# Optimization experiments

Hardware: AMD Instinct MI355X
Metric: run time of the kernel (lower is better)

Reference implementation:

```python
import jax, jax.numpy as jnp
import numpy as np


def setup_inputs() -> dict:
    key = jax.random.key(0)
    k1, k2, k3 = jax.random.split(key, 3)
    B, Cin, Cout, K, H, W = 32, 128, 128, 4, 112, 112
    x = jax.random.normal(k1, (B, Cin, H, W), dtype=jnp.float32)
    # Conv2d 1x1 weights: [K, out_ch, in_ch] (kernel dims of size 1 squeezed)
    expert_w = jax.random.normal(k2, (K, Cout, Cin), dtype=jnp.float32) * (1.0 / np.sqrt(Cin))
    gate_w = jax.random.normal(k3, (K, Cin), dtype=jnp.float32) * (1.0 / np.sqrt(Cin))
    gate_b = jnp.zeros((K,), dtype=jnp.float32)
    return {"x": x, "expert_w": expert_w, "gate_w": gate_w, "gate_b": gate_b}


def reference(x, expert_w, gate_w, gate_b):
    # Gate: global average pool -> 1x1 conv -> softmax over K
    pooled = jnp.mean(x, axis=(2, 3))                      # [B, Cin]
    logits = pooled @ gate_w.T + gate_b                    # [B, K]
    g = jax.nn.softmax(logits, axis=1)                     # [B, K]
    # Combine expert weights per sample (math-equivalent to sum_k g_k * conv_k(x))
    w_b = jnp.einsum('bk,koi->boi', g, expert_w)           # [B, Cout, Cin]
    out = jnp.einsum('boi,bihw->bohw', w_b, x)             # [B, Cout, H, W]
    return out
```

## Files before the change

### kernel.cpp

```cpp
#include <hip/hip_runtime.h>
#include <hip/hip_bf16.h>
#include <stdint.h>

#define B_    32
#define CIN   128
#define COUT  128
#define KEXP  4
#define HW_   12544

typedef __attribute__((ext_vector_type(8))) short bf16x8;
typedef __attribute__((ext_vector_type(4))) float f32x4;

static __device__ __forceinline__ short f2bf(float f) {
    uint32_t u = __builtin_bit_cast(uint32_t, f);
    u += 0x7FFFu + ((u >> 16) & 1u);
    return (short)(u >> 16);
}

__global__ __launch_bounds__(256) void pool_kernel(const float* __restrict__ x,
                                                   float* __restrict__ pooled) {
    const int row = blockIdx.x;
    const float4* __restrict__ x4 = (const float4*)(x + (size_t)row * HW_);
    const int t = threadIdx.x;
    float s = 0.f;
    for (int idx = t; idx < HW_ / 4; idx += 256) {
        float4 v = x4[idx];
        s += (v.x + v.y) + (v.z + v.w);
    }
    #pragma unroll
    for (int off = 32; off > 0; off >>= 1) s += __shfl_down(s, off, 64);
    __shared__ float wsum[4];
    if ((t & 63) == 0) wsum[t >> 6] = s;
    __syncthreads();
    if (t == 0) pooled[row] = (wsum[0] + wsum[1] + wsum[2] + wsum[3]) * (1.0f / HW_);
}

__global__ __launch_bounds__(256) void gate_kernel(const float* __restrict__ pooled,
                                                   const float* __restrict__ gate_w,
                                                   const float* __restrict__ gate_b,
                                                   const float* __restrict__ expert_w,
                                                   short* __restrict__ wmix) {
    const int b = blockIdx.x;
    const int t = threadIdx.x;
    const int wid = t >> 6, lane = t & 63;
    __shared__ float logits[KEXP];
    __shared__ float gsh[KEXP];
    {
        float p0 = pooled[b * CIN + lane];
        float p1 = pooled[b * CIN + 64 + lane];
        float s = p0 * gate_w[wid * CIN + lane] + p1 * gate_w[wid * CIN + 64 + lane];
        #pragma unroll
        for (int off = 32; off > 0; off >>= 1) s += __shfl_down(s, off, 64);
        if (lane == 0) logits[wid] = s + gate_b[wid];
    }
    __syncthreads();
    if (t == 0) {
        float m = fmaxf(fmaxf(logits[0], logits[1]), fmaxf(logits[2], logits[3]));
        float e0 = expf(logits[0] - m), e1 = expf(logits[1] - m);
        float e2 = expf(logits[2] - m), e3 = expf(logits[3] - m);
        float inv = 1.f / (e0 + e1 + e2 + e3);
        gsh[0] = e0 * inv; gsh[1] = e1 * inv; gsh[2] = e2 * inv; gsh[3] = e3 * inv;
    }
    __syncthreads();
    const float g0 = gsh[0], g1 = gsh[1], g2 = gsh[2], g3 = gsh[3];
    for (int idx = t; idx < COUT * CIN; idx += 256) {
        float w = g0 * expert_w[idx]
                + g1 * expert_w[COUT * CIN + idx]
                + g2 * expert_w[2 * COUT * CIN + idx]
                + g3 * expert_w[3 * COUT * CIN + idx];
        wmix[b * COUT * CIN + idx] = f2bf(w);
    }
}

__global__ __launch_bounds__(256) void conv_kernel(const float* __restrict__ x,
                                                   const short* __restrict__ wmix,
                                                   float* __restrict__ out) {
    __shared__ char wlds[COUT * 256];
    const int b  = blockIdx.y;
    const int p0 = blockIdx.x * 64;
    const int t  = threadIdx.x;

    {
        const uint4* __restrict__ wsrc = (const uint4*)(wmix + (size_t)b * COUT * CIN);
        #pragma unroll
        for (int pass = 0; pass < 8; ++pass) {
            int o  = (t >> 4) + pass * 16;
            int i4 = t & 15;
            uint4 v = wsrc[o * 16 + i4];
            int byte = (o * 256 + i4 * 16) ^ ((o & 7) << 4);
            *(uint4*)(wlds + byte) = v;
        }
    }

    const int wave = t >> 6;
    const int lane = t & 63;
    const int n = lane & 15;
    const int h = lane >> 4;
    const int pix = p0 + wave * 16 + n;

    const float* __restrict__ xb = x + (size_t)b * CIN * HW_ + pix;
    float xv[32];
    #pragma unroll
    for (int kk = 0; kk < 4; ++kk)
        #pragma unroll
        for (int j = 0; j < 8; ++j)
            xv[kk * 8 + j] = xb[(size_t)(kk * 32 + h * 8 + j) * HW_];

    bf16x8 bfrag[4];
    #pragma unroll
    for (int kk = 0; kk < 4; ++kk)
        #pragma unroll
        for (int j = 0; j < 8; ++j)
            bfrag[kk][j] = f2bf(xv[kk * 8 + j]);

    __syncthreads();

    f32x4 acc[8];
    #pragma unroll
    for (int ot = 0; ot < 8; ++ot) acc[ot] = (f32x4){0.f, 0.f, 0.f, 0.f};

    #pragma unroll
    for (int kk = 0; kk < 4; ++kk) {
        #pragma unroll
        for (int ot = 0; ot < 8; ++ot) {
            int o = ot * 16 + n;
            int byte = (o * 256 + kk * 64 + h * 16) ^ ((o & 7) << 4);
            bf16x8 afrag = *(const bf16x8*)(wlds + byte);
            acc[ot] = __builtin_amdgcn_mfma_f32_16x16x32_bf16(afrag, bfrag[kk], acc[ot], 0, 0, 0);
        }
    }

    float* __restrict__ ob = out + (size_t)b * COUT * HW_ + pix;
    #pragma unroll
    for (int ot = 0; ot < 8; ++ot)
        #pragma unroll
        for (int r = 0; r < 4; ++r)
            ob[(size_t)(ot * 16 + h * 4 + r) * HW_] = acc[ot][r];
}

extern "C" void kernel_launch(void* const* d_in, const int* in_sizes, int n_in,
                              void* d_out, int out_size, void* d_ws, size_t ws_size,
                              hipStream_t stream) {
    const float* x        = (const float*)d_in[0];
    const float* expert_w = (const float*)d_in[1];
    const float* gate_w   = (const float*)d_in[2];
    const float* gate_b   = (const float*)d_in[3];
    float* out = (float*)d_out;

    float* pooled = (float*)d_ws;
    short* wmix   = (short*)((char*)d_ws + 16384);

    pool_kernel<<<dim3(B_ * CIN), 256, 0, stream>>>(x, pooled);
    gate_kernel<<<dim3(B_), 256, 0, stream>>>(pooled, gate_w, gate_b, expert_w, wmix);
    conv_kernel<<<dim3(HW_ / 64, B_), 256, 0, stream>>>(x, wmix, out);
}
```

Before: 161.1 us.

## Stage x tile through LDS with float4 loads and swap MFMA operands for vector stores

After: 131.8 us. -18.2%, faster.

```diff
diff --git a/kernel.cpp b/kernel.cpp
--- a/kernel.cpp
+++ b/kernel.cpp
@@ -11,10 +11,10 @@
 typedef __attribute__((ext_vector_type(8))) short bf16x8;
 typedef __attribute__((ext_vector_type(4))) float f32x4;
 
-static __device__ __forceinline__ short f2bf(float f) {
+static __device__ __forceinline__ ushort f2bf(float f) {
     uint32_t u = __builtin_bit_cast(uint32_t, f);
     u += 0x7FFFu + ((u >> 16) & 1u);
-    return (short)(u >> 16);
+    return (ushort)(u >> 16);
 }
 
 __global__ __launch_bounds__(256) void pool_kernel(const float* __restrict__ x,
@@ -68,7 +68,7 @@
                 + g1 * expert_w[COUT * CIN + idx]
                 + g2 * expert_w[2 * COUT * CIN + idx]
                 + g3 * expert_w[3 * COUT * CIN + idx];
-        wmix[b * COUT * CIN + idx] = f2bf(w);
+        wmix[b * COUT * CIN + idx] = (short)f2bf(w);
     }
 }
 
@@ -76,6 +76,7 @@
                                                    const short* __restrict__ wmix,
                                                    float* __restrict__ out) {
     __shared__ char wlds[COUT * 256];
+    __shared__ char xlds[64 * 256];
     const int b  = blockIdx.y;
     const int p0 = blockIdx.x * 64;
     const int t  = threadIdx.x;
@@ -92,28 +93,47 @@
         }
     }
 
+    {
+        const int pg = t & 15;
+        const int cg = t >> 4;
+        #pragma unroll
+        for (int p = 0; p < 2; ++p) {
+            const int cin0 = p * 64 + cg * 4;
+            const float* xrow = x + (size_t)b * CIN * HW_ + (size_t)cin0 * HW_ + p0 + pg * 4;
+            float va[4][4];
+            #pragma unroll
+            for (int i = 0; i < 4; ++i) {
+                float4 v = *(const float4*)(xrow + (size_t)i * HW_);
+                va[i][0] = v.x; va[i][1] = v.y; va[i][2] = v.z; va[i][3] = v.w;
+            }
+            #pragma unroll
+            for (int j = 0; j < 4; ++j) {
+                const int pix = pg * 4 + j;
+                uint32_t lo = (uint32_t)f2bf(va[0][j]) | ((uint32_t)f2bf(va[1][j]) << 16);
+                uint32_t hi = (uint32_t)f2bf(va[2][j]) | ((uint32_t)f2bf(va[3][j]) << 16);
+                int byte = (pix * 256 + cin0 * 2) ^ ((pix & 7) << 4);
+                uint2 w2; w2.x = lo; w2.y = hi;
+                *(uint2*)(xlds + byte) = w2;
+            }
+        }
+    }
+
     const int wave = t >> 6;
     const int lane = t & 63;
     const int n = lane & 15;
     const int h = lane >> 4;
-    const int pix = p0 + wave * 16 + n;
-
-    const float* __restrict__ xb = x + (size_t)b * CIN * HW_ + pix;
-    float xv[32];
-    #pragma unroll
-    for (int kk = 0; kk < 4; ++kk)
-        #pragma unroll
-        for (int j = 0; j < 8; ++j)
-            xv[kk * 8 + j] = xb[(size_t)(kk * 32 + h * 8 + j) * HW_];
-
-    bf16x8 bfrag[4];
-    #pragma unroll
-    for (int kk = 0; kk < 4; ++kk)
-        #pragma unroll
-        for (int j = 0; j < 8; ++j)
-            bfrag[kk][j] = f2bf(xv[kk * 8 + j]);
 
     __syncthreads();
+
+    bf16x8 xfrag[4];
+    {
+        const int pixl = wave * 16 + n;
+        #pragma unroll
+        for (int kk = 0; kk < 4; ++kk) {
+            int byte = (pixl * 256 + kk * 64 + h * 16) ^ ((pixl & 7) << 4);
+            xfrag[kk] = *(const bf16x8*)(xlds + byte);
+        }
+    }
 
     f32x4 acc[8];
     #pragma unroll
@@ -125,17 +145,17 @@
         for (int ot = 0; ot < 8; ++ot) {
             int o = ot * 16 + n;
             int byte = (o * 256 + kk * 64 + h * 16) ^ ((o & 7) << 4);
-            bf16x8 afrag = *(const bf16x8*)(wlds + byte);
-            acc[ot] = __builtin_amdgcn_mfma_f32_16x16x32_bf16(afrag, bfrag[kk], acc[ot], 0, 0, 0);
+            bf16x8 wfrag = *(const bf16x8*)(wlds + byte);
+            acc[ot] = __builtin_amdgcn_mfma_f32_16x16x32_bf16(xfrag[kk], wfrag, acc[ot], 0, 0, 0);
         }
     }
 
-    float* __restrict__ ob = out + (size_t)b * COUT * HW_ + pix;
+    float* __restrict__ ob = out + (size_t)b * COUT * HW_ + p0 + wave * 16 + h * 4;
     #pragma unroll
-    for (int ot = 0; ot < 8; ++ot)
-        #pragma unroll
-        for (int r = 0; r < 4; ++r)
-            ob[(size_t)(ot * 16 + h * 4 + r) * HW_] = acc[ot][r];
+    for (int ot = 0; ot < 8; ++ot) {
+        int cout = ot * 16 + n;
+        __builtin_nontemporal_store(acc[ot], (f32x4*)(ob + (size_t)cout * HW_));
+    }
 }
 
 extern "C" void kernel_launch(void* const* d_in, const int* in_sizes, int n_in,
```

## Loop multiple pixel tiles per block with LDS-staged x and prefetch

Applied to the files above, without the earlier changes.

Result: faster. 133.9 us (-16.9%).

```diff
diff --git a/kernel.cpp b/kernel.cpp
--- a/kernel.cpp
+++ b/kernel.cpp
@@ -7,14 +7,15 @@
 #define COUT  128
 #define KEXP  4
 #define HW_   12544
+#define NT    4
 
 typedef __attribute__((ext_vector_type(8))) short bf16x8;
 typedef __attribute__((ext_vector_type(4))) float f32x4;
 
-static __device__ __forceinline__ short f2bf(float f) {
+static __device__ __forceinline__ ushort f2bf(float f) {
     uint32_t u = __builtin_bit_cast(uint32_t, f);
     u += 0x7FFFu + ((u >> 16) & 1u);
-    return (short)(u >> 16);
+    return (ushort)(u >> 16);
 }
 
 __global__ __launch_bounds__(256) void pool_kernel(const float* __restrict__ x,
@@ -68,17 +69,21 @@
                 + g1 * expert_w[COUT * CIN + idx]
                 + g2 * expert_w[2 * COUT * CIN + idx]
                 + g3 * expert_w[3 * COUT * CIN + idx];
-        wmix[b * COUT * CIN + idx] = f2bf(w);
+        wmix[b * COUT * CIN + idx] = (short)f2bf(w);
     }
 }
 
-__global__ __launch_bounds__(256) void conv_kernel(const float* __restrict__ x,
-                                                   const short* __restrict__ wmix,
-                                                   float* __restrict__ out) {
+__global__ __launch_bounds__(256, 4) void conv_kernel(const float* __restrict__ x,
+                                                      const short* __restrict__ wmix,
+                                                      float* __restrict__ out) {
     __shared__ char wlds[COUT * 256];
+    __shared__ char xlds[64 * 256];
     const int b  = blockIdx.y;
-    const int p0 = blockIdx.x * 64;
     const int t  = threadIdx.x;
+    const int base_p0 = blockIdx.x * (64 * NT);
+
+    const int pg  = t & 15;
+    const int cg8 = t >> 4;
 
     {
         const uint4* __restrict__ wsrc = (const uint4*)(wmix + (size_t)b * COUT * CIN);
@@ -87,55 +92,73 @@
             int o  = (t >> 4) + pass * 16;
             int i4 = t & 15;
             uint4 v = wsrc[o * 16 + i4];
-            int byte = (o * 256 + i4 * 16) ^ ((o & 7) << 4);
-            *(uint4*)(wlds + byte) = v;
+            *(uint4*)(wlds + o * 256 + ((i4 ^ (o & 15)) << 4)) = v;
         }
     }
+
+    float4 xv[8];
+    const float* __restrict__ xbase = x + (size_t)b * CIN * HW_ + (size_t)(cg8 * 8) * HW_;
+    auto load_tile = [&](int p0) {
+        const float* xr = xbase + p0 + pg * 4;
+        #pragma unroll
+        for (int i = 0; i < 8; ++i)
+            xv[i] = *(const float4*)(xr + (size_t)i * HW_);
+    };
+    auto write_tile = [&]() {
+        #pragma unroll
+        for (int j = 0; j < 4; ++j) {
+            const int pix = pg * 4 + j;
+            bf16x8 pk;
+            #pragma unroll
+            for (int i = 0; i < 8; ++i)
+                pk[i] = (short)f2bf((&xv[i].x)[j]);
+            *(bf16x8*)(xlds + pix * 256 + ((cg8 ^ (pix & 15)) << 4)) = pk;
+        }
+    };
 
     const int wave = t >> 6;
     const int lane = t & 63;
     const int n = lane & 15;
     const int h = lane >> 4;
-    const int pix = p0 + wave * 16 + n;
+    const int pixl = wave * 16 + n;
 
-    const float* __restrict__ xb = x + (size_t)b * CIN * HW_ + pix;
-    float xv[32];
-    #pragma unroll
-    for (int kk = 0; kk < 4; ++kk)
-        #pragma unroll
-        for (int j = 0; j < 8; ++j)
-            xv[kk * 8 + j] = xb[(size_t)(kk * 32 + h * 8 + j) * HW_];
-
-    bf16x8 bfrag[4];
-    #pragma unroll
-    for (int kk = 0; kk < 4; ++kk)
-        #pragma unroll
-        for (int j = 0; j < 8; ++j)
-            bfrag[kk][j] = f2bf(xv[kk * 8 + j]);
-
+    load_tile(base_p0);
+    write_tile();
     __syncthreads();
 
-    f32x4 acc[8];
-    #pragma unroll
-    for (int ot = 0; ot < 8; ++ot) acc[ot] = (f32x4){0.f, 0.f, 0.f, 0.f};
+    for (int tt = 0; tt < NT; ++tt) {
+        if (tt + 1 < NT) load_tile(base_p0 + (tt + 1) * 64);
 
-    #pragma unroll
-    for (int kk = 0; kk < 4; ++kk) {
+        bf16x8 xfrag[4];
+        #pragma unroll
+        for (int kk = 0; kk < 4; ++kk)
+            xfrag[kk] = *(const bf16x8*)(xlds + pixl * 256 + (((kk * 4 + h) ^ n) << 4));
+
+        f32x4 acc[8];
+        #pragma unroll
+        for (int ot = 0; ot < 8; ++ot) acc[ot] = (f32x4){0.f, 0.f, 0.f, 0.f};
+
         #pragma unroll
         for (int ot = 0; ot < 8; ++ot) {
-            int o = ot * 16 + n;
-            int byte = (o * 256 + kk * 64 + h * 16) ^ ((o & 7) << 4);
-            bf16x8 afrag = *(const bf16x8*)(wlds + byte);
-            acc[ot] = __builtin_amdgcn_mfma_f32_16x16x32_bf16(afrag, bfrag[kk], acc[ot], 0, 0, 0);
+            const int o = ot * 16 + n;
+            #pragma unroll
+            for (int kk = 0; kk < 4; ++kk) {
+                bf16x8 wfrag = *(const bf16x8*)(wlds + o * 256 + (((kk * 4 + h) ^ n) << 4));
+                acc[ot] = __builtin_amdgcn_mfma_f32_16x16x32_bf16(xfrag[kk], wfrag, acc[ot], 0, 0, 0);
+            }
         }
+
+        __syncthreads();
+        if (tt + 1 < NT) write_tile();
+
+        float* __restrict__ ob = out + (size_t)b * COUT * HW_ + base_p0 + tt * 64
+                               + wave * 16 + h * 4;
+        #pragma unroll
+        for (int ot = 0; ot < 8; ++ot)
+            __builtin_nontemporal_store(acc[ot], (f32x4*)(ob + (size_t)(ot * 16 + n) * HW_));
+
+        __syncthreads();
     }
-
-    float* __restrict__ ob = out + (size_t)b * COUT * HW_ + pix;
-    #pragma unroll
-    for (int ot = 0; ot < 8; ++ot)
-        #pragma unroll
-        for (int r = 0; r < 4; ++r)
-            ob[(size_t)(ot * 16 + h * 4 + r) * HW_] = acc[ot][r];
 }
 
 extern "C" void kernel_launch(void* const* d_in, const int* in_sizes, int n_in,
@@ -152,5 +175,5 @@
 
     pool_kernel<<<dim3(B_ * CIN), 256, 0, stream>>>(x, pooled);
     gate_kernel<<<dim3(B_), 256, 0, stream>>>(pooled, gate_w, gate_b, expert_w, wmix);
-    conv_kernel<<<dim3(HW_ / 64, B_), 256, 0, stream>>>(x, wmix, out);
+    conv_kernel<<<dim3(HW_ / (64 * NT), B_), 256, 0, stream>>>(x, wmix, out);
 }
```
